# Optimization experiments

Measured on AMD Instinct MI355X. Metric: run time of the kernel, lower is better.

The kernel has to match this reference:

```python
import math
import jax, jax.numpy as jnp
import numpy as np

H, D_MODEL, D_K, D_V, SEQ, BATCH = 12, 768, 64, 64, 2048, 4


def setup_inputs() -> dict:
    key = jax.random.key(0)
    k1, k2, k3, k4, k5 = jax.random.split(key, 5)
    s = math.sqrt(0.02)
    return {
        "residual": jax.random.normal(k1, (BATCH, SEQ, D_MODEL), dtype=jnp.float32),
        "W_Q": jax.random.normal(k2, (H, D_MODEL, D_K), dtype=jnp.float32) * s,
        "W_K": jax.random.normal(k3, (H, D_MODEL, D_K), dtype=jnp.float32) * s,
        "W_V": jax.random.normal(k4, (H, D_MODEL, D_V), dtype=jnp.float32) * s,
        "W_O": jax.random.normal(k5, (H * D_V, D_MODEL), dtype=jnp.float32) * s,
    }


def reference(residual, W_Q, W_K, W_V, W_O):
    B, S, _ = residual.shape
    # Projections: h=head, m=d_model, k=d_k/d_v
    Q = jnp.einsum("hmk,bsm->hbsk", W_Q, residual)
    K = jnp.einsum("hmk,bsm->hbsk", W_K, residual)
    V = jnp.einsum("hmv,bsm->hbsv", W_V, residual)
    # Scores [h, b, s_q, s_k] + additive causal mask, scaled BEFORE softmax
    QK = jnp.einsum("hbqk,hbsk->hbqs", Q, K)
    causal = jnp.triu(jnp.ones((S, S), dtype=bool), k=1)
    mask = jnp.where(causal, -jnp.inf, 0.0).astype(QK.dtype)  # broadcasts over h,b
    soft = jax.nn.softmax((QK + mask) / math.sqrt(D_K), axis=-1)
    attn = jnp.einsum("hbqs,hbsv->hbqv", soft, V)
    # [h,b,q,v] -> [b,q,h*v]
    multi_head = jnp.transpose(attn, (1, 2, 0, 3)).reshape(B, S, -1)
    return jnp.einsum("nd,bqn->bqd", W_O, multi_head)
```

## Files before the change

kernel.cpp:

```cpp
#include <hip/hip_runtime.h>

typedef _Float16 f16;
typedef __fp16 h16x2 __attribute__((ext_vector_type(2)));
typedef _Float16 f16x8 __attribute__((ext_vector_type(8)));
typedef float f32x4 __attribute__((ext_vector_type(4)));

#define H_ 12
#define B_ 4
#define S_ 2048
#define DM 768
#define DK 64
#define HBSD ((size_t)H_ * B_ * S_ * DK)

__device__ __forceinline__ f16 f2h(float f) { return (f16)f; }
__device__ __forceinline__ float max3f(float a, float b, float c) {
  return fmaxf(fmaxf(a, b), c);
}

__device__ __forceinline__ void gl_lds16(const f16* g, f16* l) {
  __builtin_amdgcn_global_load_lds(
      (const __attribute__((address_space(1))) void*)g,
      (__attribute__((address_space(3))) void*)l, 16, 0, 0);
}


__global__ __launch_bounds__(256) void cast_x_kernel(const float* __restrict__ x,
                                                     f16* __restrict__ xb, int n4) {
  int i = blockIdx.x * 256 + threadIdx.x;
  if (i < n4) {
    float4 v = ((const float4*)x)[i];
    union { f16 h[4]; uint2 u; } pk;
    pk.h[0] = f2h(v.x); pk.h[1] = f2h(v.y); pk.h[2] = f2h(v.z); pk.h[3] = f2h(v.w);
    ((uint2*)xb)[i] = pk.u;
  }
}

__global__ __launch_bounds__(256) void tcast_qkv_kernel(const float* __restrict__ WQ,
                                                        const float* __restrict__ WK,
                                                        const float* __restrict__ WV,
                                                        f16* __restrict__ Wt) {
  __shared__ float L[64][65];
  const int m0 = blockIdx.x * 64, which = blockIdx.y, h = blockIdx.z;
  const float* in = (which == 0 ? WQ : which == 1 ? WK : WV) + (size_t)h * DM * DK;
  const int t = threadIdx.x;
  const int lr = t >> 2, lc = (t & 3) * 16;
  const float* ip = in + (size_t)(m0 + lr) * DK + lc;
#pragma unroll
  for (int i = 0; i < 4; i++) {
    float4 v = *(const float4*)(ip + i * 4);
    L[lr][lc + i * 4 + 0] = v.x;
    L[lr][lc + i * 4 + 1] = v.y;
    L[lr][lc + i * 4 + 2] = v.z;
    L[lr][lc + i * 4 + 3] = v.w;
  }
  __syncthreads();
  const int oc = t >> 2, om = (t & 3) * 16;
  union { f16 hh[16]; uint4 u[2]; } pk;
#pragma unroll
  for (int jx = 0; jx < 16; jx++) pk.hh[jx] = f2h(L[om + jx][oc]);
  f16* op = Wt + ((size_t)which * DM + h * DK + oc) * DM + m0 + om;
  *(uint4*)op = pk.u[0];
  *(uint4*)(op + 8) = pk.u[1];
}

__global__ __launch_bounds__(256) void tcast_wo_kernel(const float* __restrict__ WO,
                                                       f16* __restrict__ Wt) {
  __shared__ float L[64][65];
  const int n0 = blockIdx.x * 64, d0 = blockIdx.y * 64;
  const int t = threadIdx.x;
  const int lr = t >> 2, lc = (t & 3) * 16;
  const float* ip = WO + (size_t)(n0 + lr) * DM + d0 + lc;
#pragma unroll
  for (int i = 0; i < 4; i++) {
    float4 v = *(const float4*)(ip + i * 4);
    L[lr][lc + i * 4 + 0] = v.x;
    L[lr][lc + i * 4 + 1] = v.y;
    L[lr][lc + i * 4 + 2] = v.z;
    L[lr][lc + i * 4 + 3] = v.w;
  }
  __syncthreads();
  const int oc = t >> 2, om = (t & 3) * 16;
  union { f16 hh[16]; uint4 u[2]; } pk;
#pragma unroll
  for (int jx = 0; jx < 16; jx++) pk.hh[jx] = f2h(L[om + jx][oc]);
  f16* op = Wt + (size_t)(d0 + oc) * DM + n0 + om;
  *(uint4*)op = pk.u[0];
  *(uint4*)(op + 8) = pk.u[1];
}

template <int MODE>
__global__ __launch_bounds__(256) void gemm_bt_kernel(const f16* __restrict__ A,
                                                      const f16* __restrict__ Bt,
                                                      float* __restrict__ Cf,
                                                      f16* __restrict__ Cq,
                                                      f16* __restrict__ Vt, int N) {
  constexpr int K = 768;
  __shared__ __align__(16) f16 As[2 * 128 * 32];
  __shared__ __align__(16) f16 Bs[2 * 128 * 32];
  const int t = threadIdx.x;
  const int m0 = blockIdx.y * 128, n0 = blockIdx.x * 128;
  const int lane = t & 63, wave = t >> 6;
  const int l15 = lane & 15, quad = lane >> 4;
  const int qsw = quad ^ ((l15 >> 1) & 3);
  const int m_off = (wave & 1) * 64, n_off = (wave >> 1) * 64;
  const int r0 = t >> 2, ko = ((t & 3) ^ ((t >> 3) & 3)) * 8;
  const f16* Ag0 = A + (size_t)(m0 + r0) * K + ko;
  const f16* Ag1 = A + (size_t)(m0 + r0 + 64) * K + ko;
  const f16* Bg0 = Bt + (size_t)(n0 + r0) * K + ko;
  const f16* Bg1 = Bt + (size_t)(n0 + r0 + 64) * K + ko;

  f32x4 acc[4][4];
  const f32x4 z4 = {0.f, 0.f, 0.f, 0.f};
  for (int i = 0; i < 4; i++)
    for (int j = 0; j < 4; j++) acc[i][j] = z4;

  for (int kt = 0; kt < K; kt += 64) {
    __syncthreads();
#pragma unroll
    for (int s = 0; s < 2; s++) {
      gl_lds16(Ag0 + kt + s * 32, &As[s * 4096 + t * 8]);
      gl_lds16(Ag1 + kt + s * 32, &As[s * 4096 + 2048 + t * 8]);
      gl_lds16(Bg0 + kt + s * 32, &Bs[s * 4096 + t * 8]);
      gl_lds16(Bg1 + kt + s * 32, &Bs[s * 4096 + 2048 + t * 8]);
    }
    __syncthreads();
#pragma unroll
    for (int s = 0; s < 2; s++) {
      f16x8 af[4], bfr[4];
#pragma unroll
      for (int i = 0; i < 4; i++)
        af[i] = *(const f16x8*)&As[s * 4096 + (m_off + i * 16 + l15) * 32 + qsw * 8];
#pragma unroll
      for (int i = 0; i < 4; i++)
        bfr[i] = *(const f16x8*)&Bs[s * 4096 + (n_off + i * 16 + l15) * 32 + qsw * 8];
#pragma unroll
      for (int mi = 0; mi < 4; mi++)
#pragma unroll
        for (int ni = 0; ni < 4; ni++)
          acc[mi][ni] = __builtin_amdgcn_mfma_f32_16x16x32_f16(af[mi], bfr[ni],
                                                               acc[mi][ni], 0, 0, 0);
    }
  }

  if (MODE == 0) {
#pragma unroll
    for (int mi = 0; mi < 4; mi++) {
      int row = m0 + m_off + mi * 16 + quad * 4;
#pragma unroll
      for (int ni = 0; ni < 4; ni++) {
        int col = n0 + n_off + ni * 16 + l15;
#pragma unroll
        for (int r = 0; r < 4; r++) Cf[(size_t)(row + r) * N + col] = acc[mi][ni][r];
      }
    }
  } else {
#pragma unroll
    for (int mi = 0; mi < 4; mi++) {
      int srow = m0 + m_off + mi * 16 + quad * 4;
      int bb = srow >> 11, ss = srow & 2047;
#pragma unroll
      for (int ni = 0; ni < 4; ni++) {
        int n = n0 + n_off + ni * 16 + l15;
        int which = n / DM;
        int rr = n - which * DM;
        int h = rr >> 6, kk = rr & 63;
        if (which < 2) {
#pragma unroll
          for (int r = 0; r < 4; r++) {
            size_t dst = (size_t)which * HBSD +
                         ((size_t)((h * B_ + bb) * S_) + ss + r) * DK + kk;
            Cq[dst] = f2h(acc[mi][ni][r]);
          }
        } else {
          union { f16 hh[4]; uint2 u; } pk;
#pragma unroll
          for (int r = 0; r < 4; r++) pk.hh[r] = f2h(acc[mi][ni][r]);
          *(uint2*)&Vt[((size_t)(h * B_ + bb) * DK + kk) * S_ + ss] = pk.u;
        }
      }
    }
  }
}

__global__ __launch_bounds__(256, 3) void flash_kernel(const f16* __restrict__ Qg,
                                                       const f16* __restrict__ Kg,
                                                       const f16* __restrict__ Vtg,
                                                       f16* __restrict__ MH) {
  __shared__ __align__(16) f16 Ksh[2][4096];
  __shared__ __align__(16) f16 Vsh[2][4096];
  __shared__ __align__(16) f16 Ps[4][16 * 72];

  const int t = threadIdx.x, lane = t & 63, w = t >> 6;
  const int l15 = lane & 15, quad = lane >> 4;
  const int qsw = quad ^ ((l15 >> 1) & 3);
  const int bid = blockIdx.x;
  const int xcd = bid & 7, gi = bid >> 3;
  const int hbi = gi % 6, pr = gi / 6;
  const int hb = xcd * 6 + hbi;
  const int qbA = pr, qbB = 31 - pr;
  const int h = hb >> 2, b = hb & 3;
  const size_t base = (size_t)hb * S_ * DK;
  const f16* Qp = Qg + base;
  const f16* Kp = Kg + base;
  const f16* Vp = Vtg + base;
  const float c2 = 0.18033688011f;

  f16x8 aqA[2], aqB[2];
  {
    const f16* qa = Qp + (size_t)(qbA * 64 + w * 16 + l15) * DK + quad * 8;
    aqA[0] = *(const f16x8*)(qa);
    aqA[1] = *(const f16x8*)(qa + 32);
    const f16* qb_ = Qp + (size_t)(qbB * 64 + w * 16 + l15) * DK + quad * 8;
    aqB[0] = *(const f16x8*)(qb_);
    aqB[1] = *(const f16x8*)(qb_ + 32);
  }
  const int qlaneA = qbA * 64 + w * 16 + l15;
  const int qlaneB = qbB * 64 + w * 16 + l15;

  const int srow = t >> 2, scol = ((t & 3) ^ ((t >> 3) & 3)) * 8;
  const f16* Kst = Kp + (size_t)srow * DK + scol;
  const f16* Vst = Vp + (size_t)srow * S_ + scol;

  float mA = -1e30f, lA = 0.f, mB = -1e30f, lB = 0.f;
  f32x4 oA[4], oB[4];
  const f32x4 z4 = {0.f, 0.f, 0.f, 0.f};
#pragma unroll
  for (int ni = 0; ni < 4; ni++) { oA[ni] = z4; oB[ni] = z4; }

  auto stage = [&](int buf, int kv0) {
    gl_lds16(Kst + (size_t)kv0 * DK, &Ksh[buf][t * 8]);
    gl_lds16(Kst + (size_t)kv0 * DK + 32, &Ksh[buf][2048 + t * 8]);
    gl_lds16(Vst + kv0, &Vsh[buf][t * 8]);
    gl_lds16(Vst + kv0 + 32, &Vsh[buf][2048 + t * 8]);
  };

  auto do_job = [&](int buf, const f16x8* aq, float& m_s, float& l_s, f32x4* oacc,
                    int qlane, int kv0, bool diag) {
    f32x4 sa[4];
    __builtin_amdgcn_s_setprio(1);
#pragma unroll
    for (int mi = 0; mi < 4; mi++) {
      f16x8 k0 = *(const f16x8*)&Ksh[buf][(mi * 16 + l15) * 32 + qsw * 8];
      sa[mi] = __builtin_amdgcn_mfma_f32_16x16x32_f16(k0, aq[0], z4, 0, 0, 0);
    }
#pragma unroll
    for (int mi = 0; mi < 4; mi++) {
      f16x8 k1 = *(const f16x8*)&Ksh[buf][2048 + (mi * 16 + l15) * 32 + qsw * 8];
      sa[mi] = __builtin_amdgcn_mfma_f32_16x16x32_f16(k1, aq[1], sa[mi], 0, 0, 0);
    }
    __builtin_amdgcn_s_setprio(0);

    if (diag) {
#pragma unroll
      for (int mi = 0; mi < 4; mi++)
#pragma unroll
        for (int r = 0; r < 4; r++)
          if (kv0 + mi * 16 + quad * 4 + r > qlane) sa[mi][r] = -1e30f;
    }

    float g0 = max3f(sa[0][0], sa[0][1], sa[0][2]);
    float g1 = max3f(sa[0][3], sa[1][0], sa[1][1]);
    float g2 = max3f(sa[1][2], sa[1][3], sa[2][0]);
    float g3 = max3f(sa[2][1], sa[2][2], sa[2][3]);
    float g4 = max3f(sa[3][0], sa[3][1], sa[3][2]);
    float mx = fmaxf(max3f(g0, g1, g2), max3f(g3, g4, sa[3][3]));
    mx = fmaxf(mx, __shfl_xor(mx, 16));
    mx = fmaxf(mx, __shfl_xor(mx, 32));
    float pm = mx * c2;
    if (!__all(pm <= m_s + 8.f)) {
      float m2 = fmaxf(m_s, pm);
      float alpha = __builtin_exp2f(m_s - m2);
      l_s *= alpha;
#pragma unroll
      for (int ni = 0; ni < 4; ni++)
#pragma unroll
        for (int r = 0; r < 4; r++) oacc[ni][r] *= alpha;
      m_s = m2;
    }
    const float m2 = m_s;
    float rs = 0.f;
#pragma unroll
    for (int mi = 0; mi < 4; mi++)
#pragma unroll
      for (int r = 0; r < 4; r++) {
        float p = __builtin_exp2f(fmaf(sa[mi][r], c2, -m2));
        sa[mi][r] = p;
        rs += p;
      }
    rs += __shfl_xor(rs, 16);
    rs += __shfl_xor(rs, 32);
    l_s += rs;

#pragma unroll
    for (int mi = 0; mi < 4; mi++) {
      union { h16x2 h2[2]; uint2 u; } pk;
      pk.h2[0] = __builtin_amdgcn_cvt_pkrtz(sa[mi][0], sa[mi][1]);
      pk.h2[1] = __builtin_amdgcn_cvt_pkrtz(sa[mi][2], sa[mi][3]);
      *(uint2*)&Ps[w][l15 * 72 + mi * 16 + quad * 4] = pk.u;
    }

    __builtin_amdgcn_s_setprio(1);
#pragma unroll
    for (int kc2 = 0; kc2 < 2; kc2++) {
      f16x8 ap = *(const f16x8*)&Ps[w][l15 * 72 + kc2 * 32 + quad * 8];
#pragma unroll
      for (int ni = 0; ni < 4; ni++) {
        f16x8 vf = *(const f16x8*)&Vsh[buf][kc2 * 2048 + (ni * 16 + l15) * 32 + qsw * 8];
        oacc[ni] = __builtin_amdgcn_mfma_f32_16x16x32_f16(vf, ap, oacc[ni], 0, 0, 0);
      }
    }
    __builtin_amdgcn_s_setprio(0);
  };

  stage(0, 0);
  for (int kt = 0; kt <= qbB; kt++) {
    const int kv0 = kt * 64;
    const int cur = kt & 1;
    __builtin_amdgcn_s_barrier();
    if (kt < qbB) {
      stage(cur ^ 1, kv0 + 64);
      asm volatile("s_waitcnt vmcnt(4)" ::: "memory");
    } else {
      asm volatile("s_waitcnt vmcnt(0)" ::: "memory");
    }
    __builtin_amdgcn_s_barrier();
    __builtin_amdgcn_sched_barrier(0);

    do_job(cur, aqB, mB, lB, oB, qlaneB, kv0, kt == qbB);
    if (kt <= qbA) do_job(cur, aqA, mA, lA, oA, qlaneA, kv0, kt == qbA);
  }

  {
    float linv = 1.0f / lB;
    f16* dst = MH + ((size_t)b * S_ + qlaneB) * DM + h * DK + quad * 4;
#pragma unroll
    for (int ni = 0; ni < 4; ni++) {
      union { f16 hh[4]; uint2 u; } pk;
#pragma unroll
      for (int r = 0; r < 4; r++) pk.hh[r] = f2h(oB[ni][r] * linv);
      *(uint2*)(dst + ni * 16) = pk.u;
    }
  }
  {
    float linv = 1.0f / lA;
    f16* dst = MH + ((size_t)b * S_ + qlaneA) * DM + h * DK + quad * 4;
#pragma unroll
    for (int ni = 0; ni < 4; ni++) {
      union { f16 hh[4]; uint2 u; } pk;
#pragma unroll
      for (int r = 0; r < 4; r++) pk.hh[r] = f2h(oA[ni][r] * linv);
      *(uint2*)(dst + ni * 16) = pk.u;
    }
  }
}


extern "C" void kernel_launch(void* const* d_in, const int* in_sizes, int n_in,
                              void* d_out, int out_size, void* d_ws, size_t ws_size,
                              hipStream_t stream) {
  const float* residual = (const float*)d_in[0];
  const float* WQ = (const float*)d_in[1];
  const float* WK = (const float*)d_in[2];
  const float* WV = (const float*)d_in[3];
  const float* WO = (const float*)d_in[4];
  float* out = (float*)d_out;

  char* ws = (char*)d_ws;
  size_t off = 0;
  auto alloc = [&](size_t bytes) {
    void* p = ws + off;
    off += (bytes + 255) & ~(size_t)255;
    return p;
  };
  f16* xb = (f16*)alloc((size_t)B_ * S_ * DM * 2);
  f16* wqkv = (f16*)alloc((size_t)3 * DM * DM * 2);
  f16* wot = (f16*)alloc((size_t)DM * DM * 2);
  f16* qk = (f16*)alloc(2 * HBSD * 2);
  f16* vt = (f16*)alloc(HBSD * 2);
  f16* mh = (f16*)alloc((size_t)B_ * S_ * DM * 2);

  cast_x_kernel<<<(B_ * S_ * DM / 4 + 255) / 256, 256, 0, stream>>>(residual, xb,
                                                                    B_ * S_ * DM / 4);
  tcast_qkv_kernel<<<dim3(DM / 64, 3, H_), 256, 0, stream>>>(WQ, WK, WV, wqkv);
  tcast_wo_kernel<<<dim3(DM / 64, DM / 64), 256, 0, stream>>>(WO, wot);

  gemm_bt_kernel<1><<<dim3(3 * DM / 128, B_ * S_ / 128), 256, 0, stream>>>(
      xb, wqkv, nullptr, qk, vt, 3 * DM);

  flash_kernel<<<768, 256, 0, stream>>>(qk, qk + HBSD, vt, mh);

  gemm_bt_kernel<0><<<dim3(DM / 128, B_ * S_ / 128), 256, 0, stream>>>(
      mh, wot, out, nullptr, nullptr, DM);
}
```

Measured before the change: 228.0 us.

## Remap GEMM workgroups and restructure attention KV loop without prefetch overlap

The GEMM kernel remaps the linear workgroup index so consecutive dispatches spread across eight groups, likely to improve cache locality across XCDs. The attention kernel drops the s_setprio hints around the MFMA sections. It also replaces the software-pipelined double-buffered KV loop, which prefetched the next tile while computing the current one, with a loop that loads two tiles, syncs, then computes both. This removes the load/compute overlap, so global load latency is exposed on every pair of tiles.

```diff
diff --git a/kernel.cpp b/kernel.cpp
--- a/kernel.cpp
+++ b/kernel.cpp
@@ -98,7 +98,10 @@
   __shared__ __align__(16) f16 As[2 * 128 * 32];
   __shared__ __align__(16) f16 Bs[2 * 128 * 32];
   const int t = threadIdx.x;
-  const int m0 = blockIdx.y * 128, n0 = blockIdx.x * 128;
+  const int nbx = gridDim.x, nwg = nbx * gridDim.y;
+  const int d = blockIdx.y * nbx + blockIdx.x;
+  const int wg = (d & 7) * (nwg >> 3) + (d >> 3);
+  const int m0 = (wg / nbx) * 128, n0 = (wg % nbx) * 128;
   const int lane = t & 63, wave = t >> 6;
   const int l15 = lane & 15, quad = lane >> 4;
   const int qsw = quad ^ ((l15 >> 1) & 3);
@@ -237,7 +240,6 @@
   auto do_job = [&](int buf, const f16x8* aq, float& m_s, float& l_s, f32x4* oacc,
                     int qlane, int kv0, bool diag) {
     f32x4 sa[4];
-    __builtin_amdgcn_s_setprio(1);
 #pragma unroll
     for (int mi = 0; mi < 4; mi++) {
       f16x8 k0 = *(const f16x8*)&Ksh[buf][(mi * 16 + l15) * 32 + qsw * 8];
@@ -248,7 +250,6 @@
       f16x8 k1 = *(const f16x8*)&Ksh[buf][2048 + (mi * 16 + l15) * 32 + qsw * 8];
       sa[mi] = __builtin_amdgcn_mfma_f32_16x16x32_f16(k1, aq[1], sa[mi], 0, 0, 0);
     }
-    __builtin_amdgcn_s_setprio(0);
 
     if (diag) {
 #pragma unroll
@@ -299,35 +300,36 @@
       *(uint2*)&Ps[w][l15 * 72 + mi * 16 + quad * 4] = pk.u;
     }
 
-    __builtin_amdgcn_s_setprio(1);
 #pragma unroll
     for (int kc2 = 0; kc2 < 2; kc2++) {
       f16x8 ap = *(const f16x8*)&Ps[w][l15 * 72 + kc2 * 32 + quad * 8];
 #pragma unroll
       for (int ni = 0; ni < 4; ni++) {
-        f16x8 vf = *(const f16x8*)&Vsh[buf][kc2 * 2048 + (ni * 16 + l15) * 32 + qsw * 8];
+        f16x8 vf =
+            *(const f16x8*)&Vsh[buf][kc2 * 2048 + (ni * 16 + l15) * 32 + qsw * 8];
         oacc[ni] = __builtin_amdgcn_mfma_f32_16x16x32_f16(vf, ap, oacc[ni], 0, 0, 0);
       }
     }
-    __builtin_amdgcn_s_setprio(0);
   };
 
-  stage(0, 0);
-  for (int kt = 0; kt <= qbB; kt++) {
-    const int kv0 = kt * 64;
-    const int cur = kt & 1;
-    __builtin_amdgcn_s_barrier();
-    if (kt < qbB) {
-      stage(cur ^ 1, kv0 + 64);
-      asm volatile("s_waitcnt vmcnt(4)" ::: "memory");
-    } else {
-      asm volatile("s_waitcnt vmcnt(0)" ::: "memory");
-    }
-    __builtin_amdgcn_s_barrier();
-    __builtin_amdgcn_sched_barrier(0);
-
-    do_job(cur, aqB, mB, lB, oB, qlaneB, kv0, kt == qbB);
-    if (kt <= qbA) do_job(cur, aqA, mA, lA, oA, qlaneA, kv0, kt == qbA);
+  int kt = 0;
+  while (kt + 1 <= qbB) {
+    __syncthreads();
+    stage(0, kt * 64);
+    stage(1, kt * 64 + 64);
+    __syncthreads();
+    do_job(0, aqB, mB, lB, oB, qlaneB, kt * 64, false);
+    if (kt <= qbA) do_job(0, aqA, mA, lA, oA, qlaneA, kt * 64, kt == qbA);
+    do_job(1, aqB, mB, lB, oB, qlaneB, kt * 64 + 64, kt + 1 == qbB);
+    if (kt + 1 <= qbA) do_job(1, aqA, mA, lA, oA, qlaneA, kt * 64 + 64, kt + 1 == qbA);
+    kt += 2;
+  }
+  if (kt <= qbB) {
+    __syncthreads();
+    stage(0, kt * 64);
+    __syncthreads();
+    do_job(0, aqB, mB, lB, oB, qlaneB, kt * 64, kt == qbB);
+    if (kt <= qbA) do_job(0, aqA, mA, lA, oA, qlaneA, kt * 64, kt == qbA);
   }
 
   {
```

After: 211.1 us. 7.4% less time.
